# Kernel optimization log

Measured on AMD Instinct MI355X. Metric: run time of the kernel, lower is better.

The kernel has to match this reference:

```python
import jax, jax.numpy as jnp
import numpy as np

KH = KW = 3
K = KH * KW
STRIDE = 1
PAD = 1
DIL = 1
GROUPS = 1
DG = 1  # deformable_groups
CIN = 256
COUT = 256
DC = 64  # depth_channels


def conv2d(x, w, b):
    out = jax.lax.conv_general_dilated(
        x, w, (STRIDE, STRIDE), [(PAD, PAD), (PAD, PAD)],
        rhs_dilation=(DIL, DIL), dimension_numbers=('NCHW', 'OIHW', 'NCHW'))
    return out + b[None, :, None, None]


def deform_sample(x, offset, mask):
    """Modulated deformable im2col. x:[N,C,H,W], offset:[N,DG*2*K,Ho,Wo],
    mask:[N,DG*K,Ho,Wo] or None. Returns cols [N,C,K,Ho,Wo]."""
    N, C, H, W = x.shape
    Ho = (H + 2 * PAD - (DIL * (KH - 1) + 1)) // STRIDE + 1
    Wo = (W + 2 * PAD - (DIL * (KW - 1) + 1)) // STRIDE + 1
    ky, kx = jnp.meshgrid(jnp.arange(KH), jnp.arange(KW), indexing='ij')
    # base sampling grid per kernel tap: [K,Ho,Wo]
    base_y = (jnp.arange(Ho) * STRIDE - PAD)[None, :, None] + (ky.reshape(-1) * DIL)[:, None, None]
    base_x = (jnp.arange(Wo) * STRIDE - PAD)[None, None, :] + (kx.reshape(-1) * DIL)[:, None, None]
    off = offset.reshape(N, DG, K, 2, Ho, Wo)  # [...,0]=dy, [...,1]=dx (CUDA layout)
    y = base_y[None, None].astype(x.dtype) + off[:, :, :, 0]
    xx = base_x[None, None].astype(x.dtype) + off[:, :, :, 1]
    y0 = jnp.floor(y)
    x0 = jnp.floor(xx)
    ly = y - y0
    lx = xx - x0
    y0i = y0.astype(jnp.int32)
    x0i = x0.astype(jnp.int32)
    xg = x.reshape(N, DG, C // DG, H * W)

    def gather(iy, ix):
        valid = ((iy >= 0) & (iy < H) & (ix >= 0) & (ix < W)).astype(x.dtype)
        idx = (jnp.clip(iy, 0, H - 1) * W + jnp.clip(ix, 0, W - 1)).reshape(N, DG, 1, K * Ho * Wo)
        v = jnp.take_along_axis(xg, idx, axis=3).reshape(N, DG, C // DG, K, Ho, Wo)
        return v * valid[:, :, None]

    v00 = gather(y0i, x0i)
    v01 = gather(y0i, x0i + 1)
    v10 = gather(y0i + 1, x0i)
    v11 = gather(y0i + 1, x0i + 1)
    w00 = (1 - ly) * (1 - lx)
    w01 = (1 - ly) * lx
    w10 = ly * (1 - lx)
    w11 = ly * lx
    cols = (v00 * w00[:, :, None] + v01 * w01[:, :, None]
            + v10 * w10[:, :, None] + v11 * w11[:, :, None])
    if mask is not None:
        cols = cols * mask.reshape(N, DG, 1, K, Ho, Wo)
    return cols.reshape(N, C, K, Ho, Wo)


def deform_conv2d(x, offset, mask, weight, bias):
    cols = deform_sample(x, offset, mask)  # [N,C,K,Ho,Wo]
    N, C, _, Ho, Wo = cols.shape
    Cout = weight.shape[0]
    cg = C // GROUPS
    cols = cols.reshape(N, GROUPS, cg * K, Ho * Wo)
    wg = weight.reshape(GROUPS, Cout // GROUPS, cg * K)
    out = jnp.einsum('gok,ngkp->ngop', wg, cols).reshape(N, Cout, Ho, Wo)
    return out + bias[None, :, None, None]


def setup_inputs() -> dict:
    key = jax.random.key(0)
    ks = jax.random.split(key, 8)
    x = jax.random.normal(ks[0], (4, CIN, 64, 64), dtype=jnp.float32)
    depth = jax.random.normal(ks[1], (4, DC, 64, 64), dtype=jnp.float32)
    stdv = 1.0 / np.sqrt(CIN * KH * KW)
    weight = jax.random.uniform(ks[2], (COUT, CIN // GROUPS, KH, KW), minval=-stdv, maxval=stdv, dtype=jnp.float32)
    bias = jnp.zeros((COUT,), jnp.float32)
    # offset/mask convs are zero-init in the module; use small random weights
    # so the irregular gather path is actually exercised.
    off_w = 0.05 * jax.random.normal(ks[3], (DG * 2 * K, CIN + DC, KH, KW), dtype=jnp.float32)
    off_b = 0.05 * jax.random.normal(ks[4], (DG * 2 * K,), dtype=jnp.float32)
    mask_w = 0.05 * jax.random.normal(ks[5], (DG * K, DC, KH, KW), dtype=jnp.float32)
    mask_b = 0.05 * jax.random.normal(ks[6], (DG * K,), dtype=jnp.float32)
    return {"x": x, "depth": depth, "weight": weight, "bias": bias,
            "off_w": off_w, "off_b": off_b, "mask_w": mask_w, "mask_b": mask_b}


def reference(x, depth, weight, bias, off_w, off_b, mask_w, mask_b):
    # offset = conv_offset(cat(x, depth))
    offset = conv2d(jnp.concatenate([x, depth], axis=1), off_w, off_b)
    # mask = sigmoid(DeformConv(depth, offset))  (non-modulated deform conv)
    mask = jax.nn.sigmoid(deform_conv2d(depth, offset, None, mask_w, mask_b))
    # modulated deformable conv on x
    return deform_conv2d(x, offset, mask, weight, bias)
```

## Files before the change

### kernel.cpp

```cpp
#include <hip/hip_runtime.h>


typedef __bf16 bf16x8 __attribute__((ext_vector_type(8)));
typedef float f32x4 __attribute__((ext_vector_type(4)));
typedef float float2_u __attribute__((ext_vector_type(2), aligned(4)));

__device__ __forceinline__ unsigned short f2bf(float f) {
  unsigned b = __float_as_uint(f);
  return (unsigned short)((b + 0x7fffu + ((b >> 16) & 1u)) >> 16);
}

__global__ __launch_bounds__(256) void k_prep_weight(
    const float* __restrict__ w, unsigned short* __restrict__ wbf)
{
  const int i = blockIdx.x * 256 + threadIdx.x;
  wbf[i] = f2bf(w[i]);
}

__global__ __launch_bounds__(256) void k_offset_conv(
    const float* __restrict__ x, const float* __restrict__ depth,
    const float* __restrict__ off_w, const float* __restrict__ off_b,
    float* __restrict__ offs)
{
  const int seg = blockIdx.x >> 8;
  const int nh  = blockIdx.x & 255;
  const int n = nh >> 6, ho = nh & 63;
  const int tid = threadIdx.x;
  const int lane = tid & 63;
  const int wave = tid >> 6;

  float acc[18];
#pragma unroll
  for (int i = 0; i < 18; ++i) acc[i] = 0.f;

  const int c0 = __builtin_amdgcn_readfirstlane(seg * 80 + wave * 20);

  for (int ci = 0; ci < 20; ++ci) {
    const int c = c0 + ci;
    const float* p = (c < 256) ? (x + (((n << 8) + c) << 12))
                               : (depth + (((n << 6) + (c - 256)) << 12));
    const float v0 = (ho > 0)  ? p[((ho - 1) << 6) + lane] : 0.f;
    const float v1 =             p[( ho      << 6) + lane];
    const float v2 = (ho < 63) ? p[((ho + 1) << 6) + lane] : 0.f;

    float v[9];
#pragma unroll
    for (int ky = 0; ky < 3; ++ky) {
      const float r = (ky == 0) ? v0 : ((ky == 1) ? v1 : v2);
#pragma unroll
      for (int kx = 0; kx < 3; ++kx) {
        const int src = lane + kx - 1;
        const float s = __shfl(r, src & 63);
        v[ky * 3 + kx] = (src >= 0 && src < 64) ? s : 0.f;
      }
    }
    const float* wp = off_w + c * 9;
#pragma unroll
    for (int co = 0; co < 18; ++co) {
      const float* w = wp + co * 2880;
#pragma unroll
      for (int t = 0; t < 9; ++t) acc[co] += v[t] * w[t];
    }
  }

  __shared__ float red[4][18][64];
#pragma unroll
  for (int co = 0; co < 18; ++co) red[wave][co][lane] = acc[co];
  __syncthreads();
  for (int o = tid; o < 18 * 64; o += 256) {
    const int co = o >> 6, wo = o & 63;
    float s = red[0][co][wo] + red[1][co][wo] + red[2][co][wo] + red[3][co][wo];
    if (seg == 0) s += off_b[co];
    atomicAdd(&offs[((n * 18 + co) << 12) + (ho << 6) + wo], s);
  }
}

__global__ __launch_bounds__(512) void k_mask_conv(
    const float* __restrict__ depth, const float* __restrict__ offs,
    const float* __restrict__ mask_w, const float* __restrict__ mask_b,
    float* __restrict__ mask)
{
  const int n  = blockIdx.x >> 6;
  const int ho = blockIdx.x & 63;
  const int tid  = threadIdx.x;
  const int lane = tid & 63;
  const int wave = tid >> 6;
  const int wo = lane;

  int i00[9], i01[9], i10[9], i11[9];
  float cw00[9], cw01[9], cw10[9], cw11[9];
  const float* op = offs + ((n * 18) << 12) + (ho << 6) + wo;
#pragma unroll
  for (int k = 0; k < 9; ++k) {
    const float dy = op[(2 * k) << 12];
    const float dx = op[(2 * k + 1) << 12];
    const float yy = (float)(ho - 1 + k / 3) + dy;
    const float xx = (float)(wo - 1 + k % 3) + dx;
    const float y0f = floorf(yy), x0f = floorf(xx);
    const float ly = yy - y0f, lx = xx - x0f;
    const int y0 = (int)y0f, x0 = (int)x0f;
    const int y0c = min(max(y0, 0), 63),     x0c = min(max(x0, 0), 63);
    const int y1c = min(max(y0 + 1, 0), 63), x1c = min(max(x0 + 1, 0), 63);
    const float fy0 = (y0 >= 0 && y0 < 64) ? 1.f : 0.f;
    const float fy1 = (y0 >= -1 && y0 < 63) ? 1.f : 0.f;
    const float fx0 = (x0 >= 0 && x0 < 64) ? 1.f : 0.f;
    const float fx1 = (x0 >= -1 && x0 < 63) ? 1.f : 0.f;
    i00[k] = (y0c << 6) + x0c;  i01[k] = (y0c << 6) + x1c;
    i10[k] = (y1c << 6) + x0c;  i11[k] = (y1c << 6) + x1c;
    cw00[k] = (1.f - ly) * (1.f - lx) * fy0 * fx0;
    cw01[k] = (1.f - ly) * lx * fy0 * fx1;
    cw10[k] = ly * (1.f - lx) * fy1 * fx0;
    cw11[k] = ly * lx * fy1 * fx1;
  }

  float acc[9];
#pragma unroll
  for (int i = 0; i < 9; ++i) acc[i] = 0.f;

  const int cbase = __builtin_amdgcn_readfirstlane(wave * 8);
  for (int cc = 0; cc < 8; ++cc) {
    const int c = cbase + cc;
    const float* p = depth + (((n << 6) + c) << 12);
    float val[9];
#pragma unroll
    for (int k = 0; k < 9; ++k) {
      val[k] = p[i00[k]] * cw00[k] + p[i01[k]] * cw01[k] +
               p[i10[k]] * cw10[k] + p[i11[k]] * cw11[k];
    }
    const float* wp = mask_w + c * 9;
#pragma unroll
    for (int co = 0; co < 9; ++co) {
#pragma unroll
      for (int k = 0; k < 9; ++k) acc[co] += val[k] * wp[co * 576 + k];
    }
  }

  __shared__ float red[8][9][64];
#pragma unroll
  for (int co = 0; co < 9; ++co) red[wave][co][lane] = acc[co];
  __syncthreads();
  for (int o = tid; o < 9 * 64; o += 512) {
    const int co = o >> 6, w2 = o & 63;
    float s = mask_b[co];
#pragma unroll
    for (int w = 0; w < 8; ++w) s += red[w][co][w2];
    mask[((n * 9 + co) << 12) + (ho << 6) + w2] = 1.f / (1.f + expf(-s));
  }
}

__global__ __launch_bounds__(512, 2) void k_deform_gemm(
    const float* __restrict__ x, const float* __restrict__ offs,
    const float* __restrict__ mask, const unsigned short* __restrict__ wbf,
    const float* __restrict__ bias, float* __restrict__ out)
{
  __shared__ __align__(16) unsigned short Bs[2][64][72];
  __shared__ float4 pwT[9][64];
  __shared__ int2   piT[9][64];

  const int tid = threadIdx.x;
  const int b    = blockIdx.x;
  const int xcd  = b & 7, slot = b >> 3;
  const int n    = xcd >> 1;
  const int ho0  = ((xcd & 1) << 5) + slot;
  const int pxb  = ho0 << 6;
  const int pxg0 = (n << 12) + pxb;

  for (int e = tid; e < 576; e += 512) {
    const int tap = e >> 6, pl = e & 63;
    const int pxg = pxg0 + pl;
    const int wo = pl;
    const float dy = offs[((n * 18 + 2 * tap) << 12) + pxb + pl];
    const float dx = offs[((n * 18 + 2 * tap + 1) << 12) + pxb + pl];
    const float m  = mask[((n * 9 + tap) << 12) + pxb + pl];
    (void)pxg;
    const float yy = (float)(ho0 - 1 + tap / 3) + dy;
    const float xx = (float)(wo - 1 + tap % 3) + dx;
    const float y0f = floorf(yy), x0f = floorf(xx);
    const float ly = yy - y0f, lx = xx - x0f;
    const int y0 = (int)y0f, x0 = (int)x0f;
    const int y0c = min(max(y0, 0), 63);
    const int y1c = min(max(y0 + 1, 0), 63);
    const float fy0 = (y0 >= 0 && y0 < 64) ? 1.f : 0.f;
    const float fy1 = (y0 >= -1 && y0 < 63) ? 1.f : 0.f;
    const int x0c = min(max(x0, 0), 63);
    const int x1c = min(max(x0 + 1, 0), 63);
    const int bx  = min(max(x0, 0), 62);
    const float vx0 = (x0 >= 0 && x0 < 64) ? 1.f : 0.f;
    const float vx1 = (x0 >= -1 && x0 < 63) ? 1.f : 0.f;
    const float wl = (1.f - lx) * vx0 * ((x0c == bx) ? 1.f : 0.f)
                   + lx * vx1 * ((x1c == bx) ? 1.f : 0.f);
    const float wr = (1.f - lx) * vx0 * ((x0c == bx + 1) ? 1.f : 0.f)
                   + lx * vx1 * ((x1c == bx + 1) ? 1.f : 0.f);
    const float a0 = (1.f - ly) * fy0 * m;
    const float a1 = ly * fy1 * m;
    pwT[tap][pl] = make_float4(wl * a0, wr * a0, wl * a1, wr * a1);
    piT[tap][pl] = make_int2((((y0c << 6) + bx) << 2), (((y1c << 6) + bx) << 2));
  }
  __syncthreads();

  const int pxl = tid & 63;
  const int oct = tid >> 6;
  const float* xn = x + ((long)(n << 8) << 12);

  auto sample = [&](int kc, int buf) {
    const int kk0 = kc + (oct << 3);
    int c = (int)(((unsigned)kk0 * 7282u) >> 16);
    int tap = kk0 - 9 * c;
    const char* p = (const char*)(xn + (c << 12));
    __align__(16) unsigned short v[8];
#pragma unroll
    for (int j = 0; j < 8; ++j) {
      const float4 w = pwT[tap][pxl];
      const int2 ii  = piT[tap][pxl];
      const float2_u pa = *(const float2_u*)(p + ii.x);
      const float2_u pb = *(const float2_u*)(p + ii.y);
      v[j] = f2bf(pa.x * w.x + pa.y * w.y + pb.x * w.z + pb.y * w.w);
      if (++tap == 9) { tap = 0; p += 16384; }
    }
    *(int4*)&Bs[buf][pxl][oct << 3] = *(const int4*)v;
  };

  f32x4 acc[2][4];
#pragma unroll
  for (int mt = 0; mt < 2; ++mt)
#pragma unroll
    for (int nt = 0; nt < 4; ++nt)
#pragma unroll
      for (int r = 0; r < 4; ++r) acc[mt][nt][r] = 0.f;

  sample(0, 0);
  __syncthreads();

  const int wv   = oct;
  const int lane = tid & 63;
  const int mrow = lane & 15;
  const int koct = lane >> 4;

  for (int ic = 0; ic < 36; ++ic) {
    const int kc = ic << 6;
    bf16x8 af[2][2];
#pragma unroll
    for (int mt = 0; mt < 2; ++mt)
#pragma unroll
      for (int ks = 0; ks < 2; ++ks) {
        const int row = (wv << 5) + (mt << 4) + mrow;
        const int col = kc + (ks << 5) + (koct << 3);
        af[mt][ks] = *(const bf16x8*)(wbf + row * 2304 + col);
      }

    if (ic + 1 < 36) sample((ic + 1) << 6, (ic + 1) & 1);

    const int buf = ic & 1;
#pragma unroll
    for (int ks = 0; ks < 2; ++ks)
#pragma unroll
      for (int nt = 0; nt < 4; ++nt) {
        const bf16x8 bfr =
            *(const bf16x8*)&Bs[buf][(nt << 4) + mrow][(ks << 5) + (koct << 3)];
        acc[0][nt] = __builtin_amdgcn_mfma_f32_16x16x32_bf16(af[0][ks], bfr,
                                                             acc[0][nt], 0, 0, 0);
        acc[1][nt] = __builtin_amdgcn_mfma_f32_16x16x32_bf16(af[1][ks], bfr,
                                                             acc[1][nt], 0, 0, 0);
      }
    __syncthreads();
  }

#pragma unroll
  for (int mt = 0; mt < 2; ++mt)
#pragma unroll
    for (int nt = 0; nt < 4; ++nt)
#pragma unroll
      for (int r = 0; r < 4; ++r) {
        const int co = (wv << 5) + (mt << 4) + ((lane >> 4) << 2) + r;
        const int pxg = pxb + (nt << 4) + (lane & 15);
        out[(((n << 8) + co) << 12) + pxg] = acc[mt][nt][r] + bias[co];
      }
}

extern "C" void kernel_launch(void* const* d_in, const int* in_sizes, int n_in,
                              void* d_out, int out_size, void* d_ws, size_t ws_size,
                              hipStream_t stream) {
  const float* x      = (const float*)d_in[0];
  const float* depth  = (const float*)d_in[1];
  const float* weight = (const float*)d_in[2];
  const float* bias   = (const float*)d_in[3];
  const float* off_w  = (const float*)d_in[4];
  const float* off_b  = (const float*)d_in[5];
  const float* mask_w = (const float*)d_in[6];
  const float* mask_b = (const float*)d_in[7];
  float* out = (float*)d_out;

  float* offs = (float*)d_ws;
  float* mask = offs + 294912;
  unsigned short* wbf = (unsigned short*)(mask + 147456);

  hipMemsetAsync(offs, 0, 294912 * sizeof(float), stream);
  k_prep_weight<<<2304, 256, 0, stream>>>(weight, wbf);
  k_offset_conv<<<1024, 256, 0, stream>>>(x, depth, off_w, off_b, offs);
  k_mask_conv<<<256, 512, 0, stream>>>(depth, offs, mask_w, mask_b, mask);
  k_deform_gemm<<<256, 512, 0, stream>>>(x, offs, mask, wbf, bias, out);
}
```

Baseline: 281.3 us.

## Reorder GEMM K to tap-major, split output channels, widen offset conv blocks

The weight prep now lays out the bf16 weight in tap-major K order, so the deform GEMM keeps one tap's bilinear weights and indices in registers across four K-chunks and samples eight consecutive channels per thread. The GEMM grid doubles by splitting output channels into two halves, giving more blocks but duplicating the sampling work per half. The offset conv uses 512-thread blocks with fewer channels per wave, and the mask conv precomputes paired-pixel sampling tables in shared memory instead of keeping per-thread index arrays. The intent is to cut per-sample index math and register pressure and to raise occupancy, at the cost of redundant gathers across the two channel halves.

```diff
diff --git a/kernel.cpp b/kernel.cpp
--- a/kernel.cpp
+++ b/kernel.cpp
@@ -13,11 +13,13 @@
 __global__ __launch_bounds__(256) void k_prep_weight(
     const float* __restrict__ w, unsigned short* __restrict__ wbf)
 {
-  const int i = blockIdx.x * 256 + threadIdx.x;
-  wbf[i] = f2bf(w[i]);
-}
-
-__global__ __launch_bounds__(256) void k_offset_conv(
+  const int tap = blockIdx.x;
+  const int co  = blockIdx.y;
+  const int c   = threadIdx.x;
+  wbf[co * 2304 + tap * 256 + c] = f2bf(w[(co * 256 + c) * 9 + tap]);
+}
+
+__global__ __launch_bounds__(512) void k_offset_conv(
     const float* __restrict__ x, const float* __restrict__ depth,
     const float* __restrict__ off_w, const float* __restrict__ off_b,
     float* __restrict__ offs)
@@ -33,9 +35,9 @@
 #pragma unroll
   for (int i = 0; i < 18; ++i) acc[i] = 0.f;
 
-  const int c0 = __builtin_amdgcn_readfirstlane(seg * 80 + wave * 20);
-
-  for (int ci = 0; ci < 20; ++ci) {
+  const int c0 = __builtin_amdgcn_readfirstlane(seg * 80 + wave * 10);
+
+  for (int ci = 0; ci < 10; ++ci) {
     const int c = c0 + ci;
     const float* p = (c < 256) ? (x + (((n << 8) + c) << 12))
                                : (depth + (((n << 6) + (c - 256)) << 12));
@@ -63,13 +65,15 @@
     }
   }
 
-  __shared__ float red[4][18][64];
+  __shared__ float red[8][18][64];
 #pragma unroll
   for (int co = 0; co < 18; ++co) red[wave][co][lane] = acc[co];
   __syncthreads();
-  for (int o = tid; o < 18 * 64; o += 256) {
+  for (int o = tid; o < 18 * 64; o += 512) {
     const int co = o >> 6, wo = o & 63;
-    float s = red[0][co][wo] + red[1][co][wo] + red[2][co][wo] + red[3][co][wo];
+    float s = 0.f;
+#pragma unroll
+    for (int w = 0; w < 8; ++w) s += red[w][co][wo];
     if (seg == 0) s += off_b[co];
     atomicAdd(&offs[((n * 18 + co) << 12) + (ho << 6) + wo], s);
   }
@@ -80,38 +84,44 @@
     const float* __restrict__ mask_w, const float* __restrict__ mask_b,
     float* __restrict__ mask)
 {
+  __shared__ float4 qw[9][64];
+  __shared__ int2   qi[9][64];
+  __shared__ float  red[8][9][64];
+
   const int n  = blockIdx.x >> 6;
   const int ho = blockIdx.x & 63;
   const int tid  = threadIdx.x;
   const int lane = tid & 63;
   const int wave = tid >> 6;
-  const int wo = lane;
-
-  int i00[9], i01[9], i10[9], i11[9];
-  float cw00[9], cw01[9], cw10[9], cw11[9];
-  const float* op = offs + ((n * 18) << 12) + (ho << 6) + wo;
-#pragma unroll
-  for (int k = 0; k < 9; ++k) {
-    const float dy = op[(2 * k) << 12];
-    const float dx = op[(2 * k + 1) << 12];
-    const float yy = (float)(ho - 1 + k / 3) + dy;
-    const float xx = (float)(wo - 1 + k % 3) + dx;
+
+  for (int e = tid; e < 576; e += 512) {
+    const int tap = e >> 6, pl = e & 63;
+    const float dy = offs[((n * 18 + 2 * tap) << 12) + (ho << 6) + pl];
+    const float dx = offs[((n * 18 + 2 * tap + 1) << 12) + (ho << 6) + pl];
+    const float yy = (float)(ho - 1 + tap / 3) + dy;
+    const float xx = (float)(pl - 1 + tap % 3) + dx;
     const float y0f = floorf(yy), x0f = floorf(xx);
     const float ly = yy - y0f, lx = xx - x0f;
     const int y0 = (int)y0f, x0 = (int)x0f;
-    const int y0c = min(max(y0, 0), 63),     x0c = min(max(x0, 0), 63);
-    const int y1c = min(max(y0 + 1, 0), 63), x1c = min(max(x0 + 1, 0), 63);
+    const int y0c = min(max(y0, 0), 63);
+    const int y1c = min(max(y0 + 1, 0), 63);
     const float fy0 = (y0 >= 0 && y0 < 64) ? 1.f : 0.f;
     const float fy1 = (y0 >= -1 && y0 < 63) ? 1.f : 0.f;
-    const float fx0 = (x0 >= 0 && x0 < 64) ? 1.f : 0.f;
-    const float fx1 = (x0 >= -1 && x0 < 63) ? 1.f : 0.f;
-    i00[k] = (y0c << 6) + x0c;  i01[k] = (y0c << 6) + x1c;
-    i10[k] = (y1c << 6) + x0c;  i11[k] = (y1c << 6) + x1c;
-    cw00[k] = (1.f - ly) * (1.f - lx) * fy0 * fx0;
-    cw01[k] = (1.f - ly) * lx * fy0 * fx1;
-    cw10[k] = ly * (1.f - lx) * fy1 * fx0;
-    cw11[k] = ly * lx * fy1 * fx1;
-  }
+    const int x0c = min(max(x0, 0), 63);
+    const int x1c = min(max(x0 + 1, 0), 63);
+    const int bx  = min(max(x0, 0), 62);
+    const float vx0 = (x0 >= 0 && x0 < 64) ? 1.f : 0.f;
+    const float vx1 = (x0 >= -1 && x0 < 63) ? 1.f : 0.f;
+    const float wl = (1.f - lx) * vx0 * ((x0c == bx) ? 1.f : 0.f)
+                   + lx * vx1 * ((x1c == bx) ? 1.f : 0.f);
+    const float wr = (1.f - lx) * vx0 * ((x0c == bx + 1) ? 1.f : 0.f)
+                   + lx * vx1 * ((x1c == bx + 1) ? 1.f : 0.f);
+    const float a0 = (1.f - ly) * fy0;
+    const float a1 = ly * fy1;
+    qw[tap][pl] = make_float4(wl * a0, wr * a0, wl * a1, wr * a1);
+    qi[tap][pl] = make_int2((((y0c << 6) + bx) << 2), (((y1c << 6) + bx) << 2));
+  }
+  __syncthreads();
 
   float acc[9];
 #pragma unroll
@@ -120,22 +130,20 @@
   const int cbase = __builtin_amdgcn_readfirstlane(wave * 8);
   for (int cc = 0; cc < 8; ++cc) {
     const int c = cbase + cc;
-    const float* p = depth + (((n << 6) + c) << 12);
-    float val[9];
-#pragma unroll
-    for (int k = 0; k < 9; ++k) {
-      val[k] = p[i00[k]] * cw00[k] + p[i01[k]] * cw01[k] +
-               p[i10[k]] * cw10[k] + p[i11[k]] * cw11[k];
-    }
+    const char* p = (const char*)(depth + (((n << 6) + c) << 12));
     const float* wp = mask_w + c * 9;
 #pragma unroll
-    for (int co = 0; co < 9; ++co) {
-#pragma unroll
-      for (int k = 0; k < 9; ++k) acc[co] += val[k] * wp[co * 576 + k];
-    }
-  }
-
-  __shared__ float red[8][9][64];
+    for (int tap = 0; tap < 9; ++tap) {
+      const float4 w4 = qw[tap][lane];
+      const int2 ii   = qi[tap][lane];
+      const float2_u pa = *(const float2_u*)(p + ii.x);
+      const float2_u pb = *(const float2_u*)(p + ii.y);
+      const float val = pa.x * w4.x + pa.y * w4.y + pb.x * w4.z + pb.y * w4.w;
+#pragma unroll
+      for (int co = 0; co < 9; ++co) acc[co] += val * wp[co * 576 + tap];
+    }
+  }
+
 #pragma unroll
   for (int co = 0; co < 9; ++co) red[wave][co][lane] = acc[co];
   __syncthreads();
@@ -159,22 +167,22 @@
 
   const int tid = threadIdx.x;
   const int b    = blockIdx.x;
-  const int xcd  = b & 7, slot = b >> 3;
+  const int xcd  = b & 7;
+  const int slot = b >> 3;
+  const int coh  = slot & 1;
+  const int rs   = slot >> 1;
   const int n    = xcd >> 1;
-  const int ho0  = ((xcd & 1) << 5) + slot;
+  const int ho0  = ((xcd & 1) << 5) + rs;
   const int pxb  = ho0 << 6;
-  const int pxg0 = (n << 12) + pxb;
+  const int co0  = coh << 7;
 
   for (int e = tid; e < 576; e += 512) {
     const int tap = e >> 6, pl = e & 63;
-    const int pxg = pxg0 + pl;
-    const int wo = pl;
     const float dy = offs[((n * 18 + 2 * tap) << 12) + pxb + pl];
     const float dx = offs[((n * 18 + 2 * tap + 1) << 12) + pxb + pl];
     const float m  = mask[((n * 9 + tap) << 12) + pxb + pl];
-    (void)pxg;
     const float yy = (float)(ho0 - 1 + tap / 3) + dy;
-    const float xx = (float)(wo - 1 + tap % 3) + dx;
+    const float xx = (float)(pl - 1 + tap % 3) + dx;
     const float y0f = floorf(yy), x0f = floorf(xx);
     const float ly = yy - y0f, lx = xx - x0f;
     const int y0 = (int)y0f, x0 = (int)x0f;
@@ -200,55 +208,57 @@
 
   const int pxl = tid & 63;
   const int oct = tid >> 6;
-  const float* xn = x + ((long)(n << 8) << 12);
-
-  auto sample = [&](int kc, int buf) {
-    const int kk0 = kc + (oct << 3);
-    int c = (int)(((unsigned)kk0 * 7282u) >> 16);
-    int tap = kk0 - 9 * c;
-    const char* p = (const char*)(xn + (c << 12));
+  const char* xn = (const char*)(x + ((long)(n << 8) << 12));
+
+  float4 pw;
+  int2   pi;
+
+  auto sample = [&](int s2, int buf) {
+    const char* p = xn + (((s2 << 6) + (oct << 3)) << 14);
     __align__(16) unsigned short v[8];
 #pragma unroll
     for (int j = 0; j < 8; ++j) {
-      const float4 w = pwT[tap][pxl];
-      const int2 ii  = piT[tap][pxl];
-      const float2_u pa = *(const float2_u*)(p + ii.x);
-      const float2_u pb = *(const float2_u*)(p + ii.y);
-      v[j] = f2bf(pa.x * w.x + pa.y * w.y + pb.x * w.z + pb.y * w.w);
-      if (++tap == 9) { tap = 0; p += 16384; }
+      const char* q = p + (j << 14);
+      const float2_u pa = *(const float2_u*)(q + pi.x);
+      const float2_u pb = *(const float2_u*)(q + pi.y);
+      v[j] = f2bf(pa.x * pw.x + pa.y * pw.y + pb.x * pw.z + pb.y * pw.w);
     }
     *(int4*)&Bs[buf][pxl][oct << 3] = *(const int4*)v;
   };
 
-  f32x4 acc[2][4];
-#pragma unroll
-  for (int mt = 0; mt < 2; ++mt)
-#pragma unroll
-    for (int nt = 0; nt < 4; ++nt)
-#pragma unroll
-      for (int r = 0; r < 4; ++r) acc[mt][nt][r] = 0.f;
-
+  f32x4 acc[4];
+#pragma unroll
+  for (int nt = 0; nt < 4; ++nt)
+#pragma unroll
+    for (int r = 0; r < 4; ++r) acc[nt][r] = 0.f;
+
+  pw = pwT[0][pxl];
+  pi = piT[0][pxl];
   sample(0, 0);
   __syncthreads();
 
+  const int lane = tid & 63;
   const int wv   = oct;
-  const int lane = tid & 63;
   const int mrow = lane & 15;
   const int koct = lane >> 4;
+  const int arow = co0 + (wv << 4) + mrow;
+  const unsigned short* wrow = wbf + arow * 2304;
 
   for (int ic = 0; ic < 36; ++ic) {
     const int kc = ic << 6;
-    bf16x8 af[2][2];
-#pragma unroll
-    for (int mt = 0; mt < 2; ++mt)
-#pragma unroll
-      for (int ks = 0; ks < 2; ++ks) {
-        const int row = (wv << 5) + (mt << 4) + mrow;
-        const int col = kc + (ks << 5) + (koct << 3);
-        af[mt][ks] = *(const bf16x8*)(wbf + row * 2304 + col);
+    bf16x8 af[2];
+#pragma unroll
+    for (int ks = 0; ks < 2; ++ks)
+      af[ks] = *(const bf16x8*)(wrow + kc + (ks << 5) + (koct << 3));
+
+    if (ic + 1 < 36) {
+      if (((ic + 1) & 3) == 0) {
+        const int t2 = (ic + 1) >> 2;
+        pw = pwT[t2][pxl];
+        pi = piT[t2][pxl];
       }
-
-    if (ic + 1 < 36) sample((ic + 1) << 6, (ic + 1) & 1);
+      sample((ic + 1) & 3, (ic + 1) & 1);
+    }
 
     const int buf = ic & 1;
 #pragma unroll
@@ -257,24 +267,20 @@
       for (int nt = 0; nt < 4; ++nt) {
         const bf16x8 bfr =
             *(const bf16x8*)&Bs[buf][(nt << 4) + mrow][(ks << 5) + (koct << 3)];
-        acc[0][nt] = __builtin_amdgcn_mfma_f32_16x16x32_bf16(af[0][ks], bfr,
-                                                             acc[0][nt], 0, 0, 0);
-        acc[1][nt] = __builtin_amdgcn_mfma_f32_16x16x32_bf16(af[1][ks], bfr,
-                                                             acc[1][nt], 0, 0, 0);
+        acc[nt] = __builtin_amdgcn_mfma_f32_16x16x32_bf16(af[ks], bfr,
+                                                          acc[nt], 0, 0, 0);
       }
     __syncthreads();
   }
 
 #pragma unroll
-  for (int mt = 0; mt < 2; ++mt)
-#pragma unroll
-    for (int nt = 0; nt < 4; ++nt)
-#pragma unroll
-      for (int r = 0; r < 4; ++r) {
-        const int co = (wv << 5) + (mt << 4) + ((lane >> 4) << 2) + r;
-        const int pxg = pxb + (nt << 4) + (lane & 15);
-        out[(((n << 8) + co) << 12) + pxg] = acc[mt][nt][r] + bias[co];
-      }
+  for (int nt = 0; nt < 4; ++nt)
+#pragma unroll
+    for (int r = 0; r < 4; ++r) {
+      const int co = co0 + (wv << 4) + ((lane >> 4) << 2) + r;
+      const int pxg = pxb + (nt << 4) + (lane & 15);
+      out[(((n << 8) + co) << 12) + pxg] = acc[nt][r] + bias[co];
+    }
 }
 
 extern "C" void kernel_launch(void* const* d_in, const int* in_sizes, int n_in,
@@ -295,8 +301,8 @@
   unsigned short* wbf = (unsigned short*)(mask + 147456);
 
   hipMemsetAsync(offs, 0, 294912 * sizeof(float), stream);
-  k_prep_weight<<<2304, 256, 0, stream>>>(weight, wbf);
-  k_offset_conv<<<1024, 256, 0, stream>>>(x, depth, off_w, off_b, offs);
+  k_prep_weight<<<dim3(9, 256), 256, 0, stream>>>(weight, wbf);
+  k_offset_conv<<<1024, 512, 0, stream>>>(x, depth, off_w, off_b, offs);
   k_mask_conv<<<256, 512, 0, stream>>>(depth, offs, mask_w, mask_b, mask);
-  k_deform_gemm<<<256, 512, 0, stream>>>(x, offs, mask, wbf, bias, out);
-}
+  k_deform_gemm<<<512, 512, 0, stream>>>(x, offs, mask, wbf, bias, out);
+}
```

Result: slower. 341.6 us (+21.4%).
